# Kernel tuning notes

Measured on AMD Instinct MI355X. Metric: run time of the kernel, lower is better.

Reference implementation:

```python
import jax, jax.numpy as jnp
import numpy as np

N, HW, ENC = 128, 14, 2048
V, E, D = 10000, 512, 512
MAXLEN = 32


def setup_inputs() -> dict:
    key = jax.random.key(0)
    ks = jax.random.split(key, 16)
    s = 0.02
    enc_feature = jax.random.normal(ks[0], (N, HW, HW, ENC), jnp.float32)
    enc_capt = jax.random.randint(ks[1], (N, MAXLEN), 0, V)
    capt_lengths = jax.random.randint(ks[2], (N, 1), 2, MAXLEN + 1)
    capt_lengths = capt_lengths.at[0, 0].set(MAXLEN)  # ensure max(decode_lengths)==MAXLEN-1 (static)
    rn = lambda k, sh: jax.random.normal(k, sh, jnp.float32) * s
    return dict(
        enc_feature=enc_feature, enc_capt=enc_capt, capt_lengths=capt_lengths,
        emb=rn(ks[3], (V, E)),
        W_ih=rn(ks[4], (4 * D, E + ENC)), b_ih=jnp.zeros((4 * D,), jnp.float32),
        W_hh=rn(ks[5], (4 * D, D)), b_hh=jnp.zeros((4 * D,), jnp.float32),
        W_inith=rn(ks[6], (D, ENC)), b_inith=jnp.zeros((D,), jnp.float32),
        W_initc=rn(ks[7], (D, ENC)), b_initc=jnp.zeros((D,), jnp.float32),
        W_fbeta=rn(ks[8], (ENC, D)), b_fbeta=jnp.zeros((ENC,), jnp.float32),
        W_fc=rn(ks[9], (V, D)), b_fc=jnp.zeros((V,), jnp.float32),
    )


def reference(enc_feature, enc_capt, capt_lengths, emb, W_ih, b_ih, W_hh, b_hh,
              W_inith, b_inith, W_initc, b_initc, W_fbeta, b_fbeta, W_fc, b_fc):
    n = enc_feature.shape[0]
    feat = enc_feature.reshape(n, -1, enc_feature.shape[-1])  # (N, P, ENC)
    P = feat.shape[1]
    cl = capt_lengths[:, 0]
    sort_ind = jnp.argsort(-cl)               # descending by caption length
    cl = cl[sort_ind]
    feat = feat[sort_ind]
    capt = enc_capt[sort_ind]
    embs = emb[capt]                          # (N, MAXLEN, E)
    mean_feat = feat.mean(axis=1)             # (N, ENC) - uniform attention context
    h = mean_feat @ W_inith.T + b_inith
    c = mean_feat @ W_initc.T + b_initc
    dec_len = cl - 1
    T = capt.shape[1] - 1                     # static max decode length
    mask = jnp.arange(T)[None, :] < dec_len[:, None]   # (N, T) ragged-batch mask
    xs = (jnp.swapaxes(embs[:, :T, :], 0, 1), mask.T)  # (T,N,E), (T,N)

    def step(carry, x):
        h, c = carry
        e_t, m = x
        gate = jax.nn.sigmoid(h @ W_fbeta.T + b_fbeta)          # (N, ENC)
        awe = mean_feat * gate                                   # gated attention-weighted encoding
        inp = jnp.concatenate([e_t, awe], axis=1)                # (N, E+ENC)
        g = inp @ W_ih.T + b_ih + h @ W_hh.T + b_hh              # LSTMCell gates
        i, f, gg, o = jnp.split(g, 4, axis=1)
        c_new = jax.nn.sigmoid(f) * c + jax.nn.sigmoid(i) * jnp.tanh(gg)
        h_new = jax.nn.sigmoid(o) * jnp.tanh(c_new)
        mf = m[:, None].astype(h.dtype)
        h2 = jnp.where(m[:, None], h_new, h)                     # inactive rows keep old state
        c2 = jnp.where(m[:, None], c_new, c)
        preds = (h_new @ W_fc.T + b_fc) * mf                     # dropout = identity (eval)
        return (h2, c2), (preds, mf)

    (_, _), (preds, mfs) = jax.lax.scan(step, (h, c), xs)
    predictions = jnp.swapaxes(preds, 0, 1)                      # (N, T, V)
    alphas = jnp.broadcast_to(jnp.swapaxes(mfs, 0, 1) / P, (n, T, P))  # uniform alpha, zero past len
    return predictions, capt, dec_len, alphas, sort_ind
```

## Files before the change

### kernel.cpp

```cpp
#include <hip/hip_runtime.h>
#include <hip/hip_bf16.h>
#include <math.h>

#define NB       128
#define P_HW     196
#define ENC_C    2048
#define V_SZ     10000
#define E_SZ     512
#define D_SZ     512
#define MAXLEN   32
#define T_STEPS  31

#define SZ_PRED    (128ULL * 31ULL * 10000ULL)
#define OFF_PRED   0ULL
#define OFF_CAPT   (SZ_PRED)
#define OFF_DECLEN (OFF_CAPT + 128ULL * 32ULL)
#define OFF_ALPHA  (OFF_DECLEN + 128ULL)
#define OFF_SORT   (OFF_ALPHA + 128ULL * 31ULL * 196ULL)

typedef __bf16 bf16x8 __attribute__((ext_vector_type(8)));
typedef float f32x4 __attribute__((ext_vector_type(4)));

__device__ __forceinline__ float sigf(float x) { return 1.0f / (1.0f + __expf(-x)); }

__device__ __forceinline__ unsigned short f2bf(float f) {
    unsigned int u = __float_as_uint(f);
    unsigned int r = (u + 0x7fffu + ((u >> 16) & 1u)) >> 16;
    return (unsigned short)r;
}

__global__ void sort_kernel(const int* __restrict__ capt_lengths,
                            const int* __restrict__ enc_capt,
                            int* __restrict__ sort_ind_ws,
                            int* __restrict__ dec_len_ws,
                            int* __restrict__ capt_sorted_ws,
                            float* __restrict__ dout) {
    __shared__ int cl[NB];
    int i = threadIdx.x;
    cl[i] = capt_lengths[i];
    __syncthreads();
    int my = cl[i];
    int rank = 0;
    #pragma unroll 4
    for (int j = 0; j < NB; ++j) {
        int cj = cl[j];
        rank += (cj > my) || (cj == my && j < i);
    }
    sort_ind_ws[rank] = i;
    dec_len_ws[rank]  = my - 1;
    dout[OFF_SORT + rank]   = (float)i;
    dout[OFF_DECLEN + rank] = (float)(my - 1);
    for (int t = 0; t < MAXLEN; ++t) {
        int tok = enc_capt[i * MAXLEN + t];
        capt_sorted_ws[rank * MAXLEN + t] = tok;
        dout[OFF_CAPT + rank * MAXLEN + t] = (float)tok;
    }
}

__global__ void mean_kernel(const float* __restrict__ enc_feature,
                            const int* __restrict__ sort_ind,
                            float* __restrict__ mean_feat,
                            unsigned short* __restrict__ mean16) {
    int b = blockIdx.y;
    int e = blockIdx.x * 256 + threadIdx.x;
    int src = sort_ind[b];
    const float* base = enc_feature + (size_t)src * P_HW * ENC_C + e;
    float s = 0.0f;
    #pragma unroll 4
    for (int p = 0; p < P_HW; ++p) s += base[(size_t)p * ENC_C];
    float m = s * (1.0f / (float)P_HW);
    mean_feat[(size_t)b * ENC_C + e] = m;
    mean16[(size_t)b * ENC_C + e] = f2bf(m);
}

__global__ void f32_to_bf16(const float* __restrict__ src,
                            unsigned short* __restrict__ dst, int n) {
    int i = (blockIdx.x * 256 + threadIdx.x) * 4;
    if (i < n) {
        float4 v = *reinterpret_cast<const float4*>(src + i);
        dst[i + 0] = f2bf(v.x);
        dst[i + 1] = f2bf(v.y);
        dst[i + 2] = f2bf(v.z);
        dst[i + 3] = f2bf(v.w);
    }
}

__global__ void concat_wg(const float* __restrict__ W_ih,
                          const float* __restrict__ W_hh,
                          unsigned short* __restrict__ Wg16) {
    int n = blockIdx.y;
    int col = blockIdx.x * 256 + threadIdx.x;
    float v = (col < 2560) ? W_ih[(size_t)n * 2560 + col]
                           : W_hh[(size_t)n * 512 + (col - 2560)];
    Wg16[(size_t)n * 3072 + col] = f2bf(v);
}

__global__ void bsum_kernel(const float* __restrict__ b_ih,
                            const float* __restrict__ b_hh,
                            float* __restrict__ bsum) {
    int i = blockIdx.x * 256 + threadIdx.x;
    bsum[i] = b_ih[i] + b_hh[i];
}

__global__ void embs_gather(const float* __restrict__ emb,
                            const int* __restrict__ capt_sorted,
                            unsigned short* __restrict__ embs16) {
    int idx = blockIdx.x * 256 + threadIdx.x;
    if (idx >= 31 * 128 * 512) return;
    int t = idx >> 16;
    int r = idx & 65535;
    int b = r >> 9;
    int e = r & 511;
    int tok = capt_sorted[b * MAXLEN + t];
    embs16[idx] = f2bf(emb[(size_t)tok * E_SZ + e]);
}

template <int EPI>
__global__ __launch_bounds__(64) void mfma_gemm(
    const unsigned short* __restrict__ A, int lda,
    const unsigned short* __restrict__ B, int ldb,
    int Nout, int K,
    const float* __restrict__ bias,
    float* __restrict__ Cf, unsigned short* __restrict__ Cb, int ldc,
    const float* __restrict__ meanfeat,
    const int* __restrict__ dec_len, int t) {
    int l = threadIdx.x;
    int lm = l & 15;
    int lk = (l >> 4) << 3;
    int row0 = blockIdx.y << 5;
    int col0 = blockIdx.x << 5;
    const unsigned short* pa0 = A + (size_t)(row0 + lm) * lda + lk;
    const unsigned short* pa1 = pa0 + ((size_t)lda << 4);
    int bn0 = col0 + lm;
    int bn1 = bn0 + 16;
    int cb0 = bn0 < Nout ? bn0 : Nout - 1;
    int cb1 = bn1 < Nout ? bn1 : Nout - 1;
    const unsigned short* pb0 = B + (size_t)cb0 * ldb + lk;
    const unsigned short* pb1 = B + (size_t)cb1 * ldb + lk;
    f32x4 acc00 = {0.f, 0.f, 0.f, 0.f}, acc01 = acc00, acc10 = acc00, acc11 = acc00;
    for (int k = 0; k < K; k += 32) {
        bf16x8 a0 = *(const bf16x8*)(pa0 + k);
        bf16x8 a1 = *(const bf16x8*)(pa1 + k);
        bf16x8 b0 = *(const bf16x8*)(pb0 + k);
        bf16x8 b1 = *(const bf16x8*)(pb1 + k);
        acc00 = __builtin_amdgcn_mfma_f32_16x16x32_bf16(a0, b0, acc00, 0, 0, 0);
        acc01 = __builtin_amdgcn_mfma_f32_16x16x32_bf16(a0, b1, acc01, 0, 0, 0);
        acc10 = __builtin_amdgcn_mfma_f32_16x16x32_bf16(a1, b0, acc10, 0, 0, 0);
        acc11 = __builtin_amdgcn_mfma_f32_16x16x32_bf16(a1, b1, acc11, 0, 0, 0);
    }
    int orow = (l >> 4) << 2;
    #pragma unroll
    for (int mi = 0; mi < 2; ++mi) {
        #pragma unroll
        for (int ni = 0; ni < 2; ++ni) {
            f32x4 v = (mi == 0) ? (ni == 0 ? acc00 : acc01)
                                : (ni == 0 ? acc10 : acc11);
            int col = col0 + ni * 16 + lm;
            if (col >= Nout) continue;
            #pragma unroll
            for (int r = 0; r < 4; ++r) {
                int row = row0 + mi * 16 + orow + r;
                float val = v[r] + bias[col];
                if (EPI == 0) {
                    Cf[(size_t)row * ldc + col] = val;
                } else if (EPI == 1) {
                    Cb[(size_t)row * ldc + col] =
                        f2bf(meanfeat[(size_t)row * ldc + col] * sigf(val));
                } else if (EPI == 2) {
                    bool m = t < dec_len[row];
                    Cf[OFF_PRED + ((size_t)row * 31 + t) * 10000 + col] = m ? val : 0.0f;
                } else {
                    Cb[(size_t)row * ldc + col] = f2bf(val);
                }
            }
        }
    }
}

__global__ __launch_bounds__(64) void mfma_lstm(
    const unsigned short* __restrict__ embt,
    const unsigned short* __restrict__ awe16,
    const unsigned short* __restrict__ h16,
    const unsigned short* __restrict__ Wg,
    const float* __restrict__ bsum,
    float* __restrict__ g) {
    int l = threadIdx.x;
    int lm = l & 15;
    int lk = (l >> 4) << 3;
    int row0 = blockIdx.y << 5;
    int col0 = blockIdx.x << 5;
    int r0 = row0 + lm, r1 = r0 + 16;
    const unsigned short* pe0 = embt + (size_t)r0 * 512 + lk;
    const unsigned short* pe1 = embt + (size_t)r1 * 512 + lk;
    const unsigned short* pw0 = awe16 + (size_t)r0 * 2048 + lk;
    const unsigned short* pw1 = awe16 + (size_t)r1 * 2048 + lk;
    const unsigned short* ph0 = h16 + (size_t)r0 * 512 + lk;
    const unsigned short* ph1 = h16 + (size_t)r1 * 512 + lk;
    const unsigned short* pb0 = Wg + (size_t)(col0 + lm) * 3072 + lk;
    const unsigned short* pb1 = pb0 + (size_t)16 * 3072;
    f32x4 acc00 = {0.f, 0.f, 0.f, 0.f}, acc01 = acc00, acc10 = acc00, acc11 = acc00;
    for (int k = 0; k < 3072; k += 32) {
        bf16x8 a0, a1;
        if (k < 512) {
            a0 = *(const bf16x8*)(pe0 + k);
            a1 = *(const bf16x8*)(pe1 + k);
        } else if (k < 2560) {
            a0 = *(const bf16x8*)(pw0 + (k - 512));
            a1 = *(const bf16x8*)(pw1 + (k - 512));
        } else {
            a0 = *(const bf16x8*)(ph0 + (k - 2560));
            a1 = *(const bf16x8*)(ph1 + (k - 2560));
        }
        bf16x8 b0 = *(const bf16x8*)(pb0 + k);
        bf16x8 b1 = *(const bf16x8*)(pb1 + k);
        acc00 = __builtin_amdgcn_mfma_f32_16x16x32_bf16(a0, b0, acc00, 0, 0, 0);
        acc01 = __builtin_amdgcn_mfma_f32_16x16x32_bf16(a0, b1, acc01, 0, 0, 0);
        acc10 = __builtin_amdgcn_mfma_f32_16x16x32_bf16(a1, b0, acc10, 0, 0, 0);
        acc11 = __builtin_amdgcn_mfma_f32_16x16x32_bf16(a1, b1, acc11, 0, 0, 0);
    }
    int orow = (l >> 4) << 2;
    #pragma unroll
    for (int mi = 0; mi < 2; ++mi) {
        #pragma unroll
        for (int ni = 0; ni < 2; ++ni) {
            f32x4 v = (mi == 0) ? (ni == 0 ? acc00 : acc01)
                                : (ni == 0 ? acc10 : acc11);
            int col = col0 + ni * 16 + lm;
            #pragma unroll
            for (int r = 0; r < 4; ++r) {
                int row = row0 + mi * 16 + orow + r;
                g[(size_t)row * 2048 + col] = v[r] + bsum[col];
            }
        }
    }
}

__global__ void lstm_pointwise(const float* __restrict__ g,
                               float* __restrict__ c,
                               unsigned short* __restrict__ h16,
                               unsigned short* __restrict__ hnew16,
                               const int* __restrict__ dec_len, int t) {
    int idx = blockIdx.x * 256 + threadIdx.x;
    int b = idx >> 9, d = idx & 511;
    const float* gb = g + ((size_t)b << 11);
    float gi = gb[d], gf = gb[512 + d], gg = gb[1024 + d], go = gb[1536 + d];
    float cn = sigf(gf) * c[idx] + sigf(gi) * tanhf(gg);
    float hn = sigf(go) * tanhf(cn);
    hnew16[idx] = f2bf(hn);
    if (t < dec_len[b]) {
        c[idx] = cn;
        h16[idx] = f2bf(hn);
    }
}

__global__ void alphas_kernel(const int* __restrict__ dec_len,
                              float* __restrict__ dout) {
    int idx = blockIdx.x * 256 + threadIdx.x;
    int b = idx / (31 * 196);
    int r = idx % (31 * 196);
    int t = r / 196;
    dout[OFF_ALPHA + idx] = (t < dec_len[b]) ? (1.0f / 196.0f) : 0.0f;
}

static inline char* align256(char* p) {
    return (char*)(((uintptr_t)p + 255) & ~(uintptr_t)255);
}

extern "C" void kernel_launch(void* const* d_in, const int* in_sizes, int n_in,
                              void* d_out, int out_size, void* d_ws, size_t ws_size,
                              hipStream_t stream) {
    const float* enc_feature  = (const float*)d_in[0];
    const int*   enc_capt     = (const int*)d_in[1];
    const int*   capt_lengths = (const int*)d_in[2];
    const float* emb     = (const float*)d_in[3];
    const float* W_ih    = (const float*)d_in[4];
    const float* b_ih    = (const float*)d_in[5];
    const float* W_hh    = (const float*)d_in[6];
    const float* b_hh    = (const float*)d_in[7];
    const float* W_inith = (const float*)d_in[8];
    const float* b_inith = (const float*)d_in[9];
    const float* W_initc = (const float*)d_in[10];
    const float* b_initc = (const float*)d_in[11];
    const float* W_fbeta = (const float*)d_in[12];
    const float* b_fbeta = (const float*)d_in[13];
    const float* W_fc    = (const float*)d_in[14];
    const float* b_fc    = (const float*)d_in[15];
    float* out = (float*)d_out;

    char* ws = (char*)d_ws;
    int* sort_ind    = (int*)ws;  ws += 512;
    int* dec_len     = (int*)ws;  ws += 512;
    int* capt_sorted = (int*)ws;  ws += 128 * MAXLEN * sizeof(int);
    ws = align256(ws);
    float* mean_feat = (float*)ws; ws += (size_t)128 * 2048 * 4;
    float* c         = (float*)ws; ws += (size_t)128 * 512 * 4;
    float* g         = (float*)ws; ws += (size_t)128 * 2048 * 4;
    float* bsum      = (float*)ws; ws += 2048 * 4;
    unsigned short* mean16   = (unsigned short*)ws; ws += (size_t)128 * 2048 * 2;
    unsigned short* h16      = (unsigned short*)ws; ws += (size_t)128 * 512 * 2;
    unsigned short* hnew16   = (unsigned short*)ws; ws += (size_t)128 * 512 * 2;
    unsigned short* awe16    = (unsigned short*)ws; ws += (size_t)128 * 2048 * 2;
    unsigned short* Wfb16    = (unsigned short*)ws; ws += (size_t)2048 * 512 * 2;
    unsigned short* Wg16     = (unsigned short*)ws; ws += (size_t)2048 * 3072 * 2;
    unsigned short* Wfc16    = (unsigned short*)ws; ws += (size_t)10000 * 512 * 2;
    unsigned short* Winith16 = (unsigned short*)ws; ws += (size_t)512 * 2048 * 2;
    unsigned short* Winitc16 = (unsigned short*)ws; ws += (size_t)512 * 2048 * 2;
    unsigned short* embs16   = (unsigned short*)ws; ws += (size_t)31 * 128 * 512 * 2;

    sort_kernel<<<1, 128, 0, stream>>>(capt_lengths, enc_capt, sort_ind, dec_len,
                                       capt_sorted, out);
    mean_kernel<<<dim3(8, 128), 256, 0, stream>>>(enc_feature, sort_ind,
                                                  mean_feat, mean16);

    f32_to_bf16<<<(2048 * 512 / 4 + 255) / 256, 256, 0, stream>>>(W_fbeta, Wfb16, 2048 * 512);
    f32_to_bf16<<<(10000 * 512 / 4 + 255) / 256, 256, 0, stream>>>(W_fc, Wfc16, 10000 * 512);
    f32_to_bf16<<<(512 * 2048 / 4 + 255) / 256, 256, 0, stream>>>(W_inith, Winith16, 512 * 2048);
    f32_to_bf16<<<(512 * 2048 / 4 + 255) / 256, 256, 0, stream>>>(W_initc, Winitc16, 512 * 2048);
    concat_wg<<<dim3(12, 2048), 256, 0, stream>>>(W_ih, W_hh, Wg16);
    bsum_kernel<<<8, 256, 0, stream>>>(b_ih, b_hh, bsum);
    embs_gather<<<(31 * 128 * 512 + 255) / 256, 256, 0, stream>>>(emb, capt_sorted, embs16);

    mfma_gemm<4><<<dim3(16, 4), 64, 0, stream>>>(
        mean16, 2048, Winith16, 2048, 512, 2048, b_inith,
        nullptr, h16, 512, nullptr, nullptr, 0);
    mfma_gemm<0><<<dim3(16, 4), 64, 0, stream>>>(
        mean16, 2048, Winitc16, 2048, 512, 2048, b_initc,
        c, nullptr, 512, nullptr, nullptr, 0);

    for (int t = 0; t < T_STEPS; ++t) {
        mfma_gemm<1><<<dim3(64, 4), 64, 0, stream>>>(
            h16, 512, Wfb16, 512, 2048, 512, b_fbeta,
            nullptr, awe16, 2048, mean_feat, nullptr, 0);
        mfma_lstm<<<dim3(64, 4), 64, 0, stream>>>(
            embs16 + (size_t)t * 128 * 512, awe16, h16, Wg16, bsum, g);
        lstm_pointwise<<<256, 256, 0, stream>>>(g, c, h16, hnew16, dec_len, t);
        mfma_gemm<2><<<dim3(313, 4), 64, 0, stream>>>(
            hnew16, 512, Wfc16, 512, 10000, 512, b_fc,
            out, nullptr, 0, nullptr, dec_len, t);
    }

    alphas_kernel<<<3038, 256, 0, stream>>>(dec_len, out);
}
```

Before: 2.206 ms.

## Hoist vocab projection out of recurrence and fuse LSTM gate GEMM with pointwise

```diff
diff --git a/kernel.cpp b/kernel.cpp
--- a/kernel.cpp
+++ b/kernel.cpp
@@ -110,9 +110,8 @@
     int t = idx >> 16;
     int r = idx & 65535;
     int b = r >> 9;
-    int e = r & 511;
     int tok = capt_sorted[b * MAXLEN + t];
-    embs16[idx] = f2bf(emb[(size_t)tok * E_SZ + e]);
+    embs16[idx] = f2bf(emb[(size_t)tok * E_SZ + (r & 511)]);
 }
 
 template <int EPI>
@@ -121,9 +120,7 @@
     const unsigned short* __restrict__ B, int ldb,
     int Nout, int K,
     const float* __restrict__ bias,
-    float* __restrict__ Cf, unsigned short* __restrict__ Cb, int ldc,
-    const float* __restrict__ meanfeat,
-    const int* __restrict__ dec_len, int t) {
+    float* __restrict__ Cf, unsigned short* __restrict__ Cb, int ldc) {
     int l = threadIdx.x;
     int lm = l & 15;
     int lk = (l >> 4) << 3;
@@ -131,12 +128,8 @@
     int col0 = blockIdx.x << 5;
     const unsigned short* pa0 = A + (size_t)(row0 + lm) * lda + lk;
     const unsigned short* pa1 = pa0 + ((size_t)lda << 4);
-    int bn0 = col0 + lm;
-    int bn1 = bn0 + 16;
-    int cb0 = bn0 < Nout ? bn0 : Nout - 1;
-    int cb1 = bn1 < Nout ? bn1 : Nout - 1;
-    const unsigned short* pb0 = B + (size_t)cb0 * ldb + lk;
-    const unsigned short* pb1 = B + (size_t)cb1 * ldb + lk;
+    const unsigned short* pb0 = B + (size_t)(col0 + lm) * ldb + lk;
+    const unsigned short* pb1 = pb0 + ((size_t)ldb << 4);
     f32x4 acc00 = {0.f, 0.f, 0.f, 0.f}, acc01 = acc00, acc10 = acc00, acc11 = acc00;
     for (int k = 0; k < K; k += 32) {
         bf16x8 a0 = *(const bf16x8*)(pa0 + k);
@@ -156,61 +149,40 @@
             f32x4 v = (mi == 0) ? (ni == 0 ? acc00 : acc01)
                                 : (ni == 0 ? acc10 : acc11);
             int col = col0 + ni * 16 + lm;
-            if (col >= Nout) continue;
             #pragma unroll
             for (int r = 0; r < 4; ++r) {
                 int row = row0 + mi * 16 + orow + r;
                 float val = v[r] + bias[col];
-                if (EPI == 0) {
-                    Cf[(size_t)row * ldc + col] = val;
-                } else if (EPI == 1) {
-                    Cb[(size_t)row * ldc + col] =
-                        f2bf(meanfeat[(size_t)row * ldc + col] * sigf(val));
-                } else if (EPI == 2) {
-                    bool m = t < dec_len[row];
-                    Cf[OFF_PRED + ((size_t)row * 31 + t) * 10000 + col] = m ? val : 0.0f;
-                } else {
-                    Cb[(size_t)row * ldc + col] = f2bf(val);
-                }
+                if (EPI == 0) Cf[(size_t)row * ldc + col] = val;
+                else          Cb[(size_t)row * ldc + col] = f2bf(val);
             }
         }
     }
 }
 
-__global__ __launch_bounds__(64) void mfma_lstm(
-    const unsigned short* __restrict__ embt,
-    const unsigned short* __restrict__ awe16,
+__global__ __launch_bounds__(256) void awe_fused(
     const unsigned short* __restrict__ h16,
-    const unsigned short* __restrict__ Wg,
-    const float* __restrict__ bsum,
-    float* __restrict__ g) {
-    int l = threadIdx.x;
-    int lm = l & 15;
-    int lk = (l >> 4) << 3;
+    const unsigned short* __restrict__ Wfb,
+    const float* __restrict__ b_fbeta,
+    const float* __restrict__ meanfeat,
+    unsigned short* __restrict__ awe16) {
+    __shared__ float red[2][1024];
+    int tid = threadIdx.x;
+    int w = tid >> 6, l = tid & 63;
+    int ct = w >> 1, ks = w & 1;
+    int lm = l & 15, lk = ((l >> 4) << 3);
     int row0 = blockIdx.y << 5;
-    int col0 = blockIdx.x << 5;
-    int r0 = row0 + lm, r1 = r0 + 16;
-    const unsigned short* pe0 = embt + (size_t)r0 * 512 + lk;
-    const unsigned short* pe1 = embt + (size_t)r1 * 512 + lk;
-    const unsigned short* pw0 = awe16 + (size_t)r0 * 2048 + lk;
-    const unsigned short* pw1 = awe16 + (size_t)r1 * 2048 + lk;
-    const unsigned short* ph0 = h16 + (size_t)r0 * 512 + lk;
-    const unsigned short* ph1 = h16 + (size_t)r1 * 512 + lk;
-    const unsigned short* pb0 = Wg + (size_t)(col0 + lm) * 3072 + lk;
-    const unsigned short* pb1 = pb0 + (size_t)16 * 3072;
+    int col0 = (blockIdx.x << 6) + (ct << 5);
+    int kbase = ks << 8;
+    const unsigned short* pa0 = h16 + (size_t)(row0 + lm) * 512 + kbase + lk;
+    const unsigned short* pa1 = pa0 + 16 * 512;
+    const unsigned short* pb0 = Wfb + (size_t)(col0 + lm) * 512 + kbase + lk;
+    const unsigned short* pb1 = pb0 + 16 * 512;
     f32x4 acc00 = {0.f, 0.f, 0.f, 0.f}, acc01 = acc00, acc10 = acc00, acc11 = acc00;
-    for (int k = 0; k < 3072; k += 32) {
-        bf16x8 a0, a1;
-        if (k < 512) {
-            a0 = *(const bf16x8*)(pe0 + k);
-            a1 = *(const bf16x8*)(pe1 + k);
-        } else if (k < 2560) {
-            a0 = *(const bf16x8*)(pw0 + (k - 512));
-            a1 = *(const bf16x8*)(pw1 + (k - 512));
-        } else {
-            a0 = *(const bf16x8*)(ph0 + (k - 2560));
-            a1 = *(const bf16x8*)(ph1 + (k - 2560));
-        }
+    #pragma unroll
+    for (int k = 0; k < 256; k += 32) {
+        bf16x8 a0 = *(const bf16x8*)(pa0 + k);
+        bf16x8 a1 = *(const bf16x8*)(pa1 + k);
         bf16x8 b0 = *(const bf16x8*)(pb0 + k);
         bf16x8 b1 = *(const bf16x8*)(pb1 + k);
         acc00 = __builtin_amdgcn_mfma_f32_16x16x32_bf16(a0, b0, acc00, 0, 0, 0);
@@ -219,38 +191,182 @@
         acc11 = __builtin_amdgcn_mfma_f32_16x16x32_bf16(a1, b1, acc11, 0, 0, 0);
     }
     int orow = (l >> 4) << 2;
+    if (ks == 1) {
+        #pragma unroll
+        for (int mi = 0; mi < 2; ++mi)
+            #pragma unroll
+            for (int ni = 0; ni < 2; ++ni) {
+                f32x4 v = (mi == 0) ? (ni == 0 ? acc00 : acc01)
+                                    : (ni == 0 ? acc10 : acc11);
+                #pragma unroll
+                for (int r = 0; r < 4; ++r)
+                    red[ct][(mi * 16 + orow + r) * 32 + ni * 16 + lm] = v[r];
+            }
+    }
+    __syncthreads();
+    if (ks == 0) {
+        #pragma unroll
+        for (int mi = 0; mi < 2; ++mi)
+            #pragma unroll
+            for (int ni = 0; ni < 2; ++ni) {
+                f32x4 v = (mi == 0) ? (ni == 0 ? acc00 : acc01)
+                                    : (ni == 0 ? acc10 : acc11);
+                int col = col0 + ni * 16 + lm;
+                #pragma unroll
+                for (int r = 0; r < 4; ++r) {
+                    int row = row0 + mi * 16 + orow + r;
+                    float val = v[r] + red[ct][(mi * 16 + orow + r) * 32 + ni * 16 + lm]
+                              + b_fbeta[col];
+                    awe16[(size_t)row * 2048 + col] =
+                        f2bf(meanfeat[(size_t)row * 2048 + col] * sigf(val));
+                }
+            }
+    }
+}
+
+__global__ __launch_bounds__(1024) void lstm_fused(
+    const unsigned short* __restrict__ embt,
+    const unsigned short* __restrict__ awe16,
+    const unsigned short* __restrict__ h16,
+    const unsigned short* __restrict__ Wg,
+    const float* __restrict__ bsum,
+    float* __restrict__ c,
+    unsigned short* __restrict__ h16out,
+    unsigned short* __restrict__ hnew16,
+    const int* __restrict__ dec_len, int t) {
+    __shared__ float red[12][1024];
+    __shared__ float gates[4][1024];
+    int tid = threadIdx.x;
+    int w = tid >> 6, l = tid & 63;
+    int g = w & 3, ks = w >> 2;
+    int lm = l & 15, lk = ((l >> 4) << 3);
+    int row0 = blockIdx.y << 5;
+    int d0 = blockIdx.x << 5;
+    int r0 = row0 + lm;
+    const unsigned short* pe0 = embt + (size_t)r0 * 512 + lk;
+    const unsigned short* pe1 = pe0 + 16 * 512;
+    const unsigned short* pw0 = awe16 + (size_t)r0 * 2048 + lk;
+    const unsigned short* pw1 = pw0 + 16 * 2048;
+    const unsigned short* ph0 = h16 + (size_t)r0 * 512 + lk;
+    const unsigned short* ph1 = ph0 + 16 * 512;
+    const unsigned short* pb0 = Wg + (size_t)(g * 512 + d0 + lm) * 3072 + lk;
+    const unsigned short* pb1 = pb0 + (size_t)16 * 3072;
+    f32x4 acc00 = {0.f, 0.f, 0.f, 0.f}, acc01 = acc00, acc10 = acc00, acc11 = acc00;
+    int k0 = ks * 768;
+    #pragma unroll 4
+    for (int kk = 0; kk < 768; kk += 32) {
+        int k = k0 + kk;
+        bf16x8 a0, a1;
+        if (k < 512)       { a0 = *(const bf16x8*)(pe0 + k);
+                             a1 = *(const bf16x8*)(pe1 + k); }
+        else if (k < 2560) { a0 = *(const bf16x8*)(pw0 + (k - 512));
+                             a1 = *(const bf16x8*)(pw1 + (k - 512)); }
+        else               { a0 = *(const bf16x8*)(ph0 + (k - 2560));
+                             a1 = *(const bf16x8*)(ph1 + (k - 2560)); }
+        bf16x8 b0 = *(const bf16x8*)(pb0 + k);
+        bf16x8 b1 = *(const bf16x8*)(pb1 + k);
+        acc00 = __builtin_amdgcn_mfma_f32_16x16x32_bf16(a0, b0, acc00, 0, 0, 0);
+        acc01 = __builtin_amdgcn_mfma_f32_16x16x32_bf16(a0, b1, acc01, 0, 0, 0);
+        acc10 = __builtin_amdgcn_mfma_f32_16x16x32_bf16(a1, b0, acc10, 0, 0, 0);
+        acc11 = __builtin_amdgcn_mfma_f32_16x16x32_bf16(a1, b1, acc11, 0, 0, 0);
+    }
+    int orow = (l >> 4) << 2;
+    if (ks > 0) {
+        int slot = (ks - 1) * 4 + g;
+        #pragma unroll
+        for (int mi = 0; mi < 2; ++mi)
+            #pragma unroll
+            for (int ni = 0; ni < 2; ++ni) {
+                f32x4 v = (mi == 0) ? (ni == 0 ? acc00 : acc01)
+                                    : (ni == 0 ? acc10 : acc11);
+                #pragma unroll
+                for (int r = 0; r < 4; ++r)
+                    red[slot][(mi * 16 + orow + r) * 32 + ni * 16 + lm] = v[r];
+            }
+    }
+    __syncthreads();
+    if (ks == 0) {
+        #pragma unroll
+        for (int mi = 0; mi < 2; ++mi)
+            #pragma unroll
+            for (int ni = 0; ni < 2; ++ni) {
+                f32x4 v = (mi == 0) ? (ni == 0 ? acc00 : acc01)
+                                    : (ni == 0 ? acc10 : acc11);
+                #pragma unroll
+                for (int r = 0; r < 4; ++r) {
+                    int idx = (mi * 16 + orow + r) * 32 + ni * 16 + lm;
+                    gates[g][idx] = v[r] + red[g][idx] + red[4 + g][idx] + red[8 + g][idx];
+                }
+            }
+    }
+    __syncthreads();
+    {
+        int row = tid >> 5, d = tid & 31;
+        int R = row0 + row, D = d0 + d;
+        int e = row * 32 + d;
+        float gi = gates[0][e] + bsum[D];
+        float gf = gates[1][e] + bsum[512 + D];
+        float gg = gates[2][e] + bsum[1024 + D];
+        float go = gates[3][e] + bsum[1536 + D];
+        size_t idx = (size_t)R * 512 + D;
+        float cn = sigf(gf) * c[idx] + sigf(gi) * tanhf(gg);
+        float hn = sigf(go) * tanhf(cn);
+        hnew16[idx] = f2bf(hn);
+        if (t < dec_len[R]) {
+            c[idx] = cn;
+            h16out[idx] = f2bf(hn);
+        }
+    }
+}
+
+__global__ __launch_bounds__(256) void fc_batched(
+    const unsigned short* __restrict__ hnew_all,
+    const unsigned short* __restrict__ Wfc,
+    const float* __restrict__ b_fc,
+    const int* __restrict__ dec_len,
+    float* __restrict__ out) {
+    int tid = threadIdx.x;
+    int w = tid >> 6, l = tid & 63;
+    int mi2 = w >> 1, ni2 = w & 1;
+    int lm = l & 15, lk = ((l >> 4) << 3);
+    int row0 = blockIdx.y * 64 + mi2 * 32;
+    int col0 = blockIdx.x * 64 + ni2 * 32;
+    const unsigned short* pa0 = hnew_all + (size_t)(row0 + lm) * 512 + lk;
+    const unsigned short* pa1 = pa0 + 16 * 512;
+    int bn0 = col0 + lm; if (bn0 > 9999) bn0 = 9999;
+    int bn1 = col0 + 16 + lm; if (bn1 > 9999) bn1 = 9999;
+    const unsigned short* pb0 = Wfc + (size_t)bn0 * 512 + lk;
+    const unsigned short* pb1 = Wfc + (size_t)bn1 * 512 + lk;
+    f32x4 acc00 = {0.f, 0.f, 0.f, 0.f}, acc01 = acc00, acc10 = acc00, acc11 = acc00;
+    #pragma unroll 4
+    for (int k = 0; k < 512; k += 32) {
+        bf16x8 a0 = *(const bf16x8*)(pa0 + k);
+        bf16x8 a1 = *(const bf16x8*)(pa1 + k);
+        bf16x8 b0 = *(const bf16x8*)(pb0 + k);
+        bf16x8 b1 = *(const bf16x8*)(pb1 + k);
+        acc00 = __builtin_amdgcn_mfma_f32_16x16x32_bf16(a0, b0, acc00, 0, 0, 0);
+        acc01 = __builtin_amdgcn_mfma_f32_16x16x32_bf16(a0, b1, acc01, 0, 0, 0);
+        acc10 = __builtin_amdgcn_mfma_f32_16x16x32_bf16(a1, b0, acc10, 0, 0, 0);
+        acc11 = __builtin_amdgcn_mfma_f32_16x16x32_bf16(a1, b1, acc11, 0, 0, 0);
+    }
+    int orow = (l >> 4) << 2;
     #pragma unroll
-    for (int mi = 0; mi < 2; ++mi) {
+    for (int mi = 0; mi < 2; ++mi)
         #pragma unroll
         for (int ni = 0; ni < 2; ++ni) {
             f32x4 v = (mi == 0) ? (ni == 0 ? acc00 : acc01)
                                 : (ni == 0 ? acc10 : acc11);
             int col = col0 + ni * 16 + lm;
+            if (col >= 10000) continue;
             #pragma unroll
             for (int r = 0; r < 4; ++r) {
                 int row = row0 + mi * 16 + orow + r;
-                g[(size_t)row * 2048 + col] = v[r] + bsum[col];
+                int t = row >> 7, b = row & 127;
+                float val = v[r] + b_fc[col];
+                bool m = t < dec_len[b];
+                out[OFF_PRED + ((size_t)b * 31 + t) * 10000 + col] = m ? val : 0.0f;
             }
         }
-    }
-}
-
-__global__ void lstm_pointwise(const float* __restrict__ g,
-                               float* __restrict__ c,
-                               unsigned short* __restrict__ h16,
-                               unsigned short* __restrict__ hnew16,
-                               const int* __restrict__ dec_len, int t) {
-    int idx = blockIdx.x * 256 + threadIdx.x;
-    int b = idx >> 9, d = idx & 511;
-    const float* gb = g + ((size_t)b << 11);
-    float gi = gb[d], gf = gb[512 + d], gg = gb[1024 + d], go = gb[1536 + d];
-    float cn = sigf(gf) * c[idx] + sigf(gi) * tanhf(gg);
-    float hn = sigf(go) * tanhf(cn);
-    hnew16[idx] = f2bf(hn);
-    if (t < dec_len[b]) {
-        c[idx] = cn;
-        h16[idx] = f2bf(hn);
-    }
 }
 
 __global__ void alphas_kernel(const int* __restrict__ dec_len,
@@ -294,11 +410,9 @@
     ws = align256(ws);
     float* mean_feat = (float*)ws; ws += (size_t)128 * 2048 * 4;
     float* c         = (float*)ws; ws += (size_t)128 * 512 * 4;
-    float* g         = (float*)ws; ws += (size_t)128 * 2048 * 4;
     float* bsum      = (float*)ws; ws += 2048 * 4;
     unsigned short* mean16   = (unsigned short*)ws; ws += (size_t)128 * 2048 * 2;
     unsigned short* h16      = (unsigned short*)ws; ws += (size_t)128 * 512 * 2;
-    unsigned short* hnew16   = (unsigned short*)ws; ws += (size_t)128 * 512 * 2;
     unsigned short* awe16    = (unsigned short*)ws; ws += (size_t)128 * 2048 * 2;
     unsigned short* Wfb16    = (unsigned short*)ws; ws += (size_t)2048 * 512 * 2;
     unsigned short* Wg16     = (unsigned short*)ws; ws += (size_t)2048 * 3072 * 2;
@@ -306,6 +420,7 @@
     unsigned short* Winith16 = (unsigned short*)ws; ws += (size_t)512 * 2048 * 2;
     unsigned short* Winitc16 = (unsigned short*)ws; ws += (size_t)512 * 2048 * 2;
     unsigned short* embs16   = (unsigned short*)ws; ws += (size_t)31 * 128 * 512 * 2;
+    unsigned short* hnew_all = (unsigned short*)ws; ws += (size_t)31 * 128 * 512 * 2;
 
     sort_kernel<<<1, 128, 0, stream>>>(capt_lengths, enc_capt, sort_ind, dec_len,
                                        capt_sorted, out);
@@ -321,23 +436,19 @@
     embs_gather<<<(31 * 128 * 512 + 255) / 256, 256, 0, stream>>>(emb, capt_sorted, embs16);
 
     mfma_gemm<4><<<dim3(16, 4), 64, 0, stream>>>(
-        mean16, 2048, Winith16, 2048, 512, 2048, b_inith,
-        nullptr, h16, 512, nullptr, nullptr, 0);
+        mean16, 2048, Winith16, 2048, 512, 2048, b_inith, nullptr, h16, 512);
     mfma_gemm<0><<<dim3(16, 4), 64, 0, stream>>>(
-        mean16, 2048, Winitc16, 2048, 512, 2048, b_initc,
-        c, nullptr, 512, nullptr, nullptr, 0);
+        mean16, 2048, Winitc16, 2048, 512, 2048, b_initc, c, nullptr, 512);
 
     for (int t = 0; t < T_STEPS; ++t) {
-        mfma_gemm<1><<<dim3(64, 4), 64, 0, stream>>>(
-            h16, 512, Wfb16, 512, 2048, 512, b_fbeta,
-            nullptr, awe16, 2048, mean_feat, nullptr, 0);
-        mfma_lstm<<<dim3(64, 4), 64, 0, stream>>>(
-            embs16 + (size_t)t * 128 * 512, awe16, h16, Wg16, bsum, g);
-        lstm_pointwise<<<256, 256, 0, stream>>>(g, c, h16, hnew16, dec_len, t);
-        mfma_gemm<2><<<dim3(313, 4), 64, 0, stream>>>(
-            hnew16, 512, Wfc16, 512, 10000, 512, b_fc,
-            out, nullptr, 0, nullptr, dec_len, t);
-    }
-
+        awe_fused<<<dim3(32, 4), 256, 0, stream>>>(
+            h16, Wfb16, b_fbeta, mean_feat, awe16);
+        lstm_fused<<<dim3(16, 4), 1024, 0, stream>>>(
+            embs16 + (size_t)t * 128 * 512, awe16, h16, Wg16, bsum,
+            c, h16, hnew_all + (size_t)t * 128 * 512, dec_len, t);
+    }
+
+    fc_batched<<<dim3(157, 62), 256, 0, stream>>>(
+        hnew_all, Wfc16, b_fc, dec_len, out);
     alphas_kernel<<<3038, 256, 0, stream>>>(dec_len, out);
 }
```

Result: slower. 2.341 ms (+6.1%).
